# Kernel tuning notes

Hardware: AMD Instinct MI355X
Metric: run time of the kernel (lower is better)

The kernel has to match this reference:

```python
import math
import jax, jax.numpy as jnp
import numpy as np

N, L, C_IMG, D, FF, H, NL, V = 2, 1024, 512, 512, 2048, 8, 4, 8000
EPS_ATTN = 1e-6
EPS_LN = 1e-5


def pos_enc(position, channels):
    # position: (N, L, 1) float. channels assumed even here (256 / 512).
    num = channels // 2
    log_inc = math.log(10000.0) / (num - 1)
    inv = jnp.exp(jnp.arange(num, dtype=position.dtype) * -log_inc)
    st = position * inv.reshape(1, 1, -1)  # (N, L, num)
    return jnp.concatenate([jnp.sin(st), jnp.cos(st)], -1)


def layer_norm(x, s, b):
    m = jnp.mean(x, -1, keepdims=True)
    v = jnp.mean((x - m) ** 2, -1, keepdims=True)
    return (x - m) / jnp.sqrt(v + EPS_LN) * s + b


def causal_linear_attention(x, mask, Wq, bq, Wk, bk, Wv, bv, Wo, bo):
    # x: (N, L, D), mask: (N, L, 1)
    n, l, d = x.shape
    q = (x @ Wq + bq).reshape(n, l, H, -1)
    k = (x @ Wk + bk).reshape(n, l, H, -1)
    v = (x @ Wv + bv).reshape(n, l, H, -1)
    Q = jax.nn.elu(q) + 1.0                       # elu feature map
    K = (jax.nn.elu(k) + 1.0) * mask[:, :, :, None]
    K_cum = jnp.cumsum(K, axis=1)                 # (N, L, H, dk)
    Z = 1.0 / (jnp.einsum('nlhd,nlhd->nlh', Q, K_cum) + EPS_ATTN)
    KV = jnp.cumsum(K[..., :, None] * v[..., None, :], axis=1)  # (N, L, H, dk, dv)
    out = jnp.einsum('nlhd,nlhde->nlhe', Q, KV) * Z[..., None]
    return out.reshape(n, l, d) @ Wo + bo


def encoder_layer(x, mask, p):
    (Wq, bq, Wk, bk, Wv, bv, Wo, bo, W1, b1, W2, b2, s1, be1, s2, be2) = p
    x = x + causal_linear_attention(x, mask, Wq, bq, Wk, bk, Wv, bv, Wo, bo)
    x = layer_norm(x, s1, be1)
    y = jax.nn.gelu(x @ W1 + b1, approximate=False) @ W2 + b2
    return layer_norm(x + y, s2, be2)


def setup_inputs() -> dict:
    key = jax.random.key(0)
    ks = iter(jax.random.split(key, 64))

    def p(shape):
        return jax.random.normal(next(ks), shape, dtype=jnp.float32) * 0.02

    x_img = jax.random.normal(next(ks), (N, L, C_IMG), dtype=jnp.float32)
    x_txt = jax.random.randint(next(ks), (N, L), 0, V)
    pos = jnp.broadcast_to(jnp.arange(L, dtype=jnp.float32)[None, :, None], (N, L, 1))
    pos_r = jnp.floor(pos / 32.0)
    pos_c = jnp.mod(pos, 32.0)
    pos_t = pos
    first_half = (jnp.arange(L) < L // 2).astype(jnp.float32)[None, :, None]
    mask_img = jnp.broadcast_to(first_half, (N, L, 1))
    mask_txt = 1.0 - mask_img

    inp = dict(x_img=x_img, x_txt=x_txt, mask_img=mask_img, mask_txt=mask_txt,
               pos_r=pos_r, pos_c=pos_c, pos_t=pos_t,
               W_ei=p((C_IMG, D)), b_ei=jnp.zeros((D,)),
               emb_txt=p((V, D)),
               Wq=p((NL, D, D)), bq=jnp.zeros((NL, D)),
               Wk=p((NL, D, D)), bk=jnp.zeros((NL, D)),
               Wv=p((NL, D, D)), bv=jnp.zeros((NL, D)),
               Wo=p((NL, D, D)), bo=jnp.zeros((NL, D)),
               W1=p((NL, D, FF)), b1=jnp.zeros((NL, FF)),
               W2=p((NL, FF, D)), b2=jnp.zeros((NL, D)),
               ln1_s=jnp.ones((NL, D)), ln1_b=jnp.zeros((NL, D)),
               ln2_s=jnp.ones((NL, D)), ln2_b=jnp.zeros((NL, D)),
               W_pi=p((D, C_IMG)), b_pi=jnp.zeros((C_IMG,)),
               W_pt=p((D, V)), b_pt=jnp.zeros((V,)))
    return inp


def reference(x_img, x_txt, mask_img, mask_txt, pos_r, pos_c, pos_t,
              W_ei, b_ei, emb_txt,
              Wq, bq, Wk, bk, Wv, bv, Wo, bo, W1, b1, W2, b2,
              ln1_s, ln1_b, ln2_s, ln2_b, W_pi, b_pi, W_pt, b_pt):
    x_mask = mask_img + mask_txt  # (N, L, 1)
    # image embedding
    half = D // 2
    x_pos = jnp.concatenate([pos_enc(pos_r, half), pos_enc(pos_c, D - half)], -1)
    x_emb_img = ((x_img @ W_ei + b_ei) + x_pos) * mask_img
    # text embedding
    x_emb_txt = (emb_txt[x_txt] + pos_enc(pos_t, D)) * mask_txt
    x = x_emb_img + x_emb_txt
    for i in range(NL):
        p = (Wq[i], bq[i], Wk[i], bk[i], Wv[i], bv[i], Wo[i], bo[i],
             W1[i], b1[i], W2[i], b2[i], ln1_s[i], ln1_b[i], ln2_s[i], ln2_b[i])
        x = encoder_layer(x, x_mask, p)
    logit_img = x @ W_pi + b_pi
    logit_txt = x @ W_pt + b_pt
    return (logit_img, logit_txt)
```

## Files before the change

### kernel.cpp

```cpp
#include <hip/hip_runtime.h>
#include <hip/hip_bf16.h>
#include <math.h>

#define NB 2
#define LSEQ 1024
#define DM 512
#define FFD 2048
#define NHEAD 8
#define DKH 64
#define NLAYER 4
#define VOCAB 8000
#define NCHUNK 16
#define NROWS (NB * LSEQ)
#define QS 1536
#define NHEADCAT 8512
#define NHEADPAD 8576

#define OP_NONE 0
#define OP_GELU 2
#define OP_QKV  3
#define OP_PART 4
#define OP_HEAD 5

typedef __attribute__((ext_vector_type(8))) short short8;
typedef __attribute__((ext_vector_type(4))) float f32x4;
typedef __hip_bfloat16 bf16;

__device__ __forceinline__ void cast_tile(
    const float* __restrict__ s, bf16* __restrict__ d, int K, int N,
    int n0, int k0, int tid)
{
    __shared__ float tile[32][33];
    const int r  = tid >> 3;
    const int c4 = (tid & 7) * 4;
    const int n  = n0 + c4;
    float4 v = make_float4(0.f, 0.f, 0.f, 0.f);
    if (n < N)
        v = *(const float4*)(s + (size_t)(k0 + r) * N + n);
    tile[r][c4 + 0] = v.x; tile[r][c4 + 1] = v.y;
    tile[r][c4 + 2] = v.z; tile[r][c4 + 3] = v.w;
    __syncthreads();
    const int nr = tid >> 3;
    const int kc = (tid & 7) * 4;
    bf16 o[4];
    o[0] = __float2bfloat16(tile[kc + 0][nr]);
    o[1] = __float2bfloat16(tile[kc + 1][nr]);
    o[2] = __float2bfloat16(tile[kc + 2][nr]);
    o[3] = __float2bfloat16(tile[kc + 3][nr]);
    *(unsigned long long*)(d + (size_t)(n0 + nr) * K + k0 + kc) =
        *(const unsigned long long*)o;
    __syncthreads();
}

#define CO_QKVO 0
#define CO_W1   4096
#define CO_W2   8192
#define CO_WEI  12288
#define CO_WPI  12544
#define CO_WPT  12800
#define CO_XIMG 16832
#define CO_QKVB 17856
#define CO_HB   17860
#define CO_END  17894

__global__ __launch_bounds__(256) void setup_all(
    const float* __restrict__ Wq, const float* __restrict__ Wk,
    const float* __restrict__ Wv, const float* __restrict__ Wo,
    const float* __restrict__ W1, const float* __restrict__ W2,
    const float* __restrict__ Wei, const float* __restrict__ Wpi,
    const float* __restrict__ Wpt,
    bf16* __restrict__ QKVt, bf16* __restrict__ Wot,
    bf16* __restrict__ W1t, bf16* __restrict__ W2t,
    bf16* __restrict__ Weit, bf16* __restrict__ Whead,
    const float* __restrict__ x_img, bf16* __restrict__ ximgh,
    const float* __restrict__ bq, const float* __restrict__ bk,
    const float* __restrict__ bv, float* __restrict__ qkvB,
    const float* __restrict__ bpi, const float* __restrict__ bpt,
    float* __restrict__ hb)
{
    const int id = blockIdx.x;
    const int tid = threadIdx.x;

    if (id < CO_W1) {
        const int rel = id;
        const int z = rel >> 8, t = rel & 255;
        const int layer = z >> 2, which = z & 3;
        const float* src = (which == 0 ? Wq : which == 1 ? Wk : which == 2 ? Wv : Wo)
                           + (size_t)layer * 262144;
        bf16* dst = (which < 3)
            ? (QKVt + (size_t)layer * 786432 + (size_t)which * 262144)
            : (Wot + (size_t)layer * 262144);
        cast_tile(src, dst, 512, 512, (t & 15) * 32, (t >> 4) * 32, tid);
    } else if (id < CO_W2) {
        const int rel = id - CO_W1;
        const int z = rel >> 10, t = rel & 1023;
        cast_tile(W1 + (size_t)z * 1048576, W1t + (size_t)z * 1048576,
                  512, 2048, (t & 63) * 32, (t >> 6) * 32, tid);
    } else if (id < CO_WEI) {
        const int rel = id - CO_W2;
        const int z = rel >> 10, t = rel & 1023;
        cast_tile(W2 + (size_t)z * 1048576, W2t + (size_t)z * 1048576,
                  2048, 512, (t & 15) * 32, (t >> 4) * 32, tid);
    } else if (id < CO_WPI) {
        const int t = id - CO_WEI;
        cast_tile(Wei, Weit, 512, 512, (t & 15) * 32, (t >> 4) * 32, tid);
    } else if (id < CO_WPT) {
        const int t = id - CO_WPI;
        cast_tile(Wpi, Whead, 512, 512, (t & 15) * 32, (t >> 4) * 32, tid);
    } else if (id < CO_XIMG) {
        const int t = id - CO_WPT;
        cast_tile(Wpt, Whead + 262144, 512, VOCAB,
                  (t % 252) * 32, (t / 252) * 32, tid);
    } else if (id < CO_QKVB) {
        const int i = (id - CO_XIMG) * 256 + tid;
        const float4 v = *(const float4*)(x_img + (size_t)i * 4);
        ximgh[(size_t)i * 4 + 0] = __float2bfloat16(v.x);
        ximgh[(size_t)i * 4 + 1] = __float2bfloat16(v.y);
        ximgh[(size_t)i * 4 + 2] = __float2bfloat16(v.z);
        ximgh[(size_t)i * 4 + 3] = __float2bfloat16(v.w);
    } else if (id < CO_HB) {
        const int z = id - CO_QKVB;
        for (int j = tid; j < QS; j += 256) {
            float v;
            if (j < 512)       v = bq[z * DM + j];
            else if (j < 1024) v = bk[z * DM + j - 512];
            else               v = bv[z * DM + j - 1024];
            qkvB[z * QS + j] = v;
        }
    } else {
        const int j = (id - CO_HB) * 256 + tid;
        if (j < NHEADPAD)
            hb[j] = (j < 512) ? bpi[j] : (j < NHEADCAT ? bpt[j - 512] : 0.f);
    }
}

template<int BM, int BN>
__global__ __launch_bounds__(256) void gemm16(
    const bf16* __restrict__ A, const bf16* __restrict__ Bt,
    const float* __restrict__ bias, const float* __restrict__ res,
    float* __restrict__ outF, float* __restrict__ outF2,
    bf16* __restrict__ outH,
    int M, int K, int Nout, int op, int kslab)
{
    constexpr int WM = BM / 2, WN = BN / 2, MI = WM / 16, NI = WN / 16;
    constexpr int LA = BM / 64, LB = BN / 64;
    constexpr int NL = LA + LB;
    __shared__ bf16 As[3][BM * 32];
    __shared__ bf16 Bs[3][BN * 32];
    const int tid = threadIdx.x;
    const int lane = tid & 63;
    const int wave = tid >> 6;
    const int wm = (wave >> 1) * WM, wn = (wave & 1) * WN;

    int bxi = blockIdx.x, byi = blockIdx.y;
    if (op == OP_HEAD) {
        const int gx = gridDim.x;
        const int nwg = gx * gridDim.y;
        int flat = byi * gx + bxi;
        const int q = nwg >> 3, r = nwg & 7;
        const int xcd = flat & 7, lid = flat >> 3;
        flat = (xcd < r ? xcd * (q + 1) : r * (q + 1) + (xcd - r) * q) + lid;
        bxi = flat % gx;
        byi = flat / gx;
    }
    const int bm = (op == OP_HEAD ? bxi : blockIdx.y) * BM;
    const int bn = (op == OP_HEAD ? byi : blockIdx.x) * BN;
    const int l16 = lane & 15, quad = lane >> 4;

    const int rA = tid >> 2;
    const int c8 = (tid & 3) << 3;

    f32x4 acc[MI][NI];
    #pragma unroll
    for (int i = 0; i < MI; ++i)
        #pragma unroll
        for (int j = 0; j < NI; ++j) acc[i][j] = (f32x4){0.f, 0.f, 0.f, 0.f};

    const bf16* gA = A  + (size_t)(bm + rA) * K + c8;
    const bf16* gB = Bt + (size_t)(bn + rA) * K + c8;
    const int ldsWaveOff = wave * 1024;

    const int kStart = blockIdx.z * kslab;
    const int kEnd = kStart + kslab;

    auto stage = [&](int buf, int k0) {
        #pragma unroll
        for (int i = 0; i < LA; ++i)
            __builtin_amdgcn_global_load_lds(
                (const __attribute__((address_space(1))) void*)(gA + (size_t)i * 64 * K + k0),
                (__attribute__((address_space(3))) void*)((char*)As[buf] + i * 4096 + ldsWaveOff),
                16, 0, 0);
        #pragma unroll
        for (int i = 0; i < LB; ++i)
            __builtin_amdgcn_global_load_lds(
                (const __attribute__((address_space(1))) void*)(gB + (size_t)i * 64 * K + k0),
                (__attribute__((address_space(3))) void*)((char*)Bs[buf] + i * 4096 + ldsWaveOff),
                16, 0, 0);
    };

    stage(0, kStart);
    if (kStart + 32 < kEnd) stage(1, kStart + 32);
    int cur = 0;
    for (int k0 = kStart; k0 < kEnd; k0 += 32) {
        const int k2 = k0 + 64;
        if (k2 < kEnd) {
            int nb = cur + 2; if (nb >= 3) nb -= 3;
            stage(nb, k2);
            asm volatile("s_waitcnt vmcnt(%0)" :: "n"(2 * NL) : "memory");
        } else if (k0 + 32 < kEnd) {
            asm volatile("s_waitcnt vmcnt(%0)" :: "n"(NL) : "memory");
        } else {
            asm volatile("s_waitcnt vmcnt(0)" ::: "memory");
        }
        __builtin_amdgcn_s_barrier();
        short8 a[MI], b[NI];
        #pragma unroll
        for (int i = 0; i < MI; ++i)
            a[i] = *(const short8*)(As[cur] + (size_t)(wm + i * 16 + l16) * 32 + quad * 8);
        #pragma unroll
        for (int j = 0; j < NI; ++j)
            b[j] = *(const short8*)(Bs[cur] + (size_t)(wn + j * 16 + l16) * 32 + quad * 8);
        #pragma unroll
        for (int i = 0; i < MI; ++i)
            #pragma unroll
            for (int j = 0; j < NI; ++j)
                acc[i][j] = __builtin_amdgcn_mfma_f32_16x16x32_bf16(
                    a[i], b[j], acc[i][j], 0, 0, 0);
        __builtin_amdgcn_s_barrier();
        ++cur; if (cur >= 3) cur -= 3;
    }

    if (op == OP_PART) {
        float* dst = outF + (size_t)blockIdx.z * (size_t)M * Nout;
        #pragma unroll
        for (int j = 0; j < NI; ++j) {
            const int col = bn + wn + j * 16 + l16;
            #pragma unroll
            for (int i = 0; i < MI; ++i)
                #pragma unroll
                for (int r = 0; r < 4; ++r) {
                    const int row = bm + wm + i * 16 + quad * 4 + r;
                    dst[(size_t)row * Nout + col] = acc[i][j][r];
                }
        }
        return;
    }
    if (op == OP_HEAD) {
        #pragma unroll
        for (int j = 0; j < NI; ++j) {
            const int col = bn + wn + j * 16 + l16;
            const bool cok = (col < NHEADCAT);
            const float bz = cok ? bias[col] : 0.f;
            #pragma unroll
            for (int i = 0; i < MI; ++i)
                #pragma unroll
                for (int r = 0; r < 4; ++r) {
                    const int row = bm + wm + i * 16 + quad * 4 + r;
                    const float v = acc[i][j][r] + bz;
                    if (cok) {
                        if (col < 512) outF[(size_t)row * 512 + col] = v;
                        else           outF2[(size_t)row * VOCAB + (col - 512)] = v;
                    }
                }
        }
        return;
    }

    #pragma unroll
    for (int j = 0; j < NI; ++j) {
        const int col = bn + wn + j * 16 + l16;
        const bool cok = (col < Nout);
        const float bz = cok ? bias[col] : 0.f;
        #pragma unroll
        for (int i = 0; i < MI; ++i) {
            #pragma unroll
            for (int r = 0; r < 4; ++r) {
                const int row = bm + wm + i * 16 + quad * 4 + r;
                float v = acc[i][j][r] + bz;
                if (op == OP_GELU)      v = 0.5f * v * (1.f + erff(v * 0.70710678118654752f));
                else if (op == OP_QKV && col < 1024) v = (v > 0.f) ? v + 1.f : expf(v);
                if (cok) {
                    if (res)  v += res[(size_t)row * Nout + col];
                    if (outF) outF[(size_t)row * Nout + col] = v;
                    if (outH) outH[(size_t)row * Nout + col] = __float2bfloat16(v);
                }
            }
        }
    }
}

__global__ __launch_bounds__(256) void embed_k(
    const float* __restrict__ gI, const int* __restrict__ xt,
    const float* __restrict__ emb,
    const float* __restrict__ mi, const float* __restrict__ mt,
    const float* __restrict__ pr, const float* __restrict__ pc,
    const float* __restrict__ pt, float* __restrict__ X, bf16* __restrict__ Xh)
{
    const int row = blockIdx.x;
    const float prv = pr[row], pcv = pc[row], ptv = pt[row];
    const float miv = mi[row], mtv = mt[row];
    const int tok = xt[row];
    const float LOG1E4 = 9.2103403719761836f;
    const float LI127 = LOG1E4 / 127.f;
    const float LI255 = LOG1E4 / 255.f;

    for (int d = threadIdx.x; d < DM; d += 256) {
        float ip;
        if (d < 128)       ip = sinf(prv * expf(-(float)d * LI127));
        else if (d < 256)  ip = cosf(prv * expf(-(float)(d - 128) * LI127));
        else if (d < 384)  ip = sinf(pcv * expf(-(float)(d - 256) * LI127));
        else               ip = cosf(pcv * expf(-(float)(d - 384) * LI127));
        float tp;
        if (d < 256) tp = sinf(ptv * expf(-(float)d * LI255));
        else         tp = cosf(ptv * expf(-(float)(d - 256) * LI255));
        const float v = miv * (gI[(size_t)row * DM + d] + ip)
                      + mtv * (emb[(size_t)tok * DM + d] + tp);
        X[(size_t)row * DM + d] = v;
        Xh[(size_t)row * DM + d] = __float2bfloat16(v);
    }
}

__global__ __launch_bounds__(256) void ln_red(
    const float* __restrict__ P, int nP,
    const float* __restrict__ bias, const float* __restrict__ res,
    const float* __restrict__ g, const float* __restrict__ b,
    float* __restrict__ out, bf16* __restrict__ outh)
{
    const int row = blockIdx.x;
    const int tid = threadIdx.x;
    const int lane = tid & 63, wv = tid >> 6;
    const size_t base = (size_t)row * DM;
    float x0 = res[base + tid] + bias[tid];
    float x1 = res[base + tid + 256] + bias[tid + 256];
    for (int p = 0; p < nP; ++p) {
        x0 += P[(size_t)p * 1048576 + base + tid];
        x1 += P[(size_t)p * 1048576 + base + tid + 256];
    }
    __shared__ float redA[4];
    __shared__ float redB[4];
    float s = x0 + x1;
    #pragma unroll
    for (int off = 32; off > 0; off >>= 1) s += __shfl_down(s, off);
    if (lane == 0) redA[wv] = s;
    __syncthreads();
    const float mean = (redA[0] + redA[1] + redA[2] + redA[3]) * (1.f / (float)DM);
    const float d0 = x0 - mean, d1 = x1 - mean;
    float v = d0 * d0 + d1 * d1;
    #pragma unroll
    for (int off = 32; off > 0; off >>= 1) v += __shfl_down(v, off);
    if (lane == 0) redB[wv] = v;
    __syncthreads();
    const float var = (redB[0] + redB[1] + redB[2] + redB[3]) * (1.f / (float)DM);
    const float rstd = rsqrtf(var + 1e-5f);
    const float y0 = d0 * rstd * g[tid] + b[tid];
    const float y1 = d1 * rstd * g[tid + 256] + b[tid + 256];
    out[base + tid]        = y0;
    out[base + tid + 256]  = y1;
    outh[base + tid]       = __float2bfloat16(y0);
    outh[base + tid + 256] = __float2bfloat16(y1);
}

__global__ __launch_bounds__(256) void attn_kv(
    const float* __restrict__ Kp, const float* __restrict__ Vp,
    float* __restrict__ S, float* __restrict__ ks)
{
    const int c = blockIdx.x, h = blockIdx.y, n = blockIdx.z;
    const int tid = threadIdx.x;
    __shared__ float sK[64][64], sV[64][64], part[4][64];

    const int lr = tid >> 4;
    const int c4 = (tid & 15) * 4;
    #pragma unroll
    for (int it = 0; it < 4; ++it) {
        const int row = it * 16 + lr;
        const size_t gb = ((size_t)(n * LSEQ + c * 64 + row)) * QS + h * DKH + c4;
        *(float4*)&sK[row][c4] = *(const float4*)(Kp + gb);
        *(float4*)&sV[row][c4] = *(const float4*)(Vp + gb);
    }
    __syncthreads();

    const int e = tid & 63, dq = tid >> 6;
    float s[16] = {};
    for (int l = 0; l < 64; ++l) {
        const float vv = sV[l][e];
        const float4 k0 = *(const float4*)&sK[l][dq * 16 + 0];
        const float4 k1 = *(const float4*)&sK[l][dq * 16 + 4];
        const float4 k2 = *(const float4*)&sK[l][dq * 16 + 8];
        const float4 k3 = *(const float4*)&sK[l][dq * 16 + 12];
        s[0]  = fmaf(k0.x, vv, s[0]);  s[1]  = fmaf(k0.y, vv, s[1]);
        s[2]  = fmaf(k0.z, vv, s[2]);  s[3]  = fmaf(k0.w, vv, s[3]);
        s[4]  = fmaf(k1.x, vv, s[4]);  s[5]  = fmaf(k1.y, vv, s[5]);
        s[6]  = fmaf(k1.z, vv, s[6]);  s[7]  = fmaf(k1.w, vv, s[7]);
        s[8]  = fmaf(k2.x, vv, s[8]);  s[9]  = fmaf(k2.y, vv, s[9]);
        s[10] = fmaf(k2.z, vv, s[10]); s[11] = fmaf(k2.w, vv, s[11]);
        s[12] = fmaf(k3.x, vv, s[12]); s[13] = fmaf(k3.y, vv, s[13]);
        s[14] = fmaf(k3.z, vv, s[14]); s[15] = fmaf(k3.w, vv, s[15]);
    }
    const size_t sb = (((size_t)(n * NHEAD + h)) * NCHUNK + c) * 4096;
    #pragma unroll
    for (int i = 0; i < 16; ++i) S[sb + (size_t)(dq * 16 + i) * 64 + e] = s[i];

    float kp = 0.f;
    #pragma unroll
    for (int i = 0; i < 16; ++i) kp += sK[dq * 16 + i][e];
    part[dq][e] = kp;
    __syncthreads();
    if (tid < 64)
        ks[(((size_t)(n * NHEAD + h)) * NCHUNK + c) * 64 + tid] =
            part[0][tid] + part[1][tid] + part[2][tid] + part[3][tid];
}

__global__ __launch_bounds__(256) void attn_out(
    const float* __restrict__ QKV, const float* __restrict__ S,
    const float* __restrict__ ks, bf16* __restrict__ O)
{
    const int c = blockIdx.x, h = blockIdx.y, n = blockIdx.z;
    const int tid = threadIdx.x;
    __shared__ float sQt[64][64];
    __shared__ float sKt[64][64];
    __shared__ float sV [64][64];
    __shared__ float sS [64][64];
    __shared__ float sPt[64][65];
    __shared__ float skp[64];

    const size_t nhS = ((size_t)(n * NHEAD + h)) * NCHUNK * 4096;
    const size_t nhK = ((size_t)(n * NHEAD + h)) * NCHUNK * 64;

    {
        float4 aS[4] = {};
        for (int cc = 0; cc < c; ++cc) {
            const float* Sc = S + nhS + (size_t)cc * 4096;
            #pragma unroll
            for (int i = 0; i < 4; ++i) {
                const float4 t = *(const float4*)(Sc + i * 1024 + tid * 4);
                aS[i].x += t.x; aS[i].y += t.y; aS[i].z += t.z; aS[i].w += t.w;
            }
        }
        float* sSf = &sS[0][0];
        #pragma unroll
        for (int i = 0; i < 4; ++i)
            *(float4*)(sSf + i * 1024 + tid * 4) = aS[i];
        if (tid < 64) {
            float kp = 0.f;
            for (int cc = 0; cc < c; ++cc) kp += ks[nhK + cc * 64 + tid];
            skp[tid] = kp;
        }
    }

    const int lr = tid >> 4;
    const int c4 = (tid & 15) * 4;
    #pragma unroll
    for (int it = 0; it < 4; ++it) {
        const int row = it * 16 + lr;
        const size_t gb = ((size_t)(n * LSEQ + c * 64 + row)) * QS + h * DKH + c4;
        const float4 q4 = *(const float4*)(QKV + gb);
        const float4 k4 = *(const float4*)(QKV + gb + 512);
        const float4 v4 = *(const float4*)(QKV + gb + 1024);
        sQt[c4 + 0][row] = q4.x; sQt[c4 + 1][row] = q4.y;
        sQt[c4 + 2][row] = q4.z; sQt[c4 + 3][row] = q4.w;
        sKt[c4 + 0][row] = k4.x; sKt[c4 + 1][row] = k4.y;
        sKt[c4 + 2][row] = k4.z; sKt[c4 + 3][row] = k4.w;
        *(float4*)&sV[row][c4] = v4;
    }
    __syncthreads();

    const int m4 = (tid & 15) * 4;
    const int lg = tid >> 4;
    {
        float p[4][4] = {};
        for (int d = 0; d < 64; ++d) {
            const float4 k4 = *(const float4*)&sKt[d][m4];
            const float4 q4 = *(const float4*)&sQt[d][lg * 4];
            p[0][0] = fmaf(q4.x, k4.x, p[0][0]); p[0][1] = fmaf(q4.x, k4.y, p[0][1]);
            p[0][2] = fmaf(q4.x, k4.z, p[0][2]); p[0][3] = fmaf(q4.x, k4.w, p[0][3]);
            p[1][0] = fmaf(q4.y, k4.x, p[1][0]); p[1][1] = fmaf(q4.y, k4.y, p[1][1]);
            p[1][2] = fmaf(q4.y, k4.z, p[1][2]); p[1][3] = fmaf(q4.y, k4.w, p[1][3]);
            p[2][0] = fmaf(q4.z, k4.x, p[2][0]); p[2][1] = fmaf(q4.z, k4.y, p[2][1]);
            p[2][2] = fmaf(q4.z, k4.z, p[2][2]); p[2][3] = fmaf(q4.z, k4.w, p[2][3]);
            p[3][0] = fmaf(q4.w, k4.x, p[3][0]); p[3][1] = fmaf(q4.w, k4.y, p[3][1]);
            p[3][2] = fmaf(q4.w, k4.z, p[3][2]); p[3][3] = fmaf(q4.w, k4.w, p[3][3]);
        }
        #pragma unroll
        for (int jj = 0; jj < 4; ++jj)
            #pragma unroll
            for (int j = 0; j < 4; ++j)
                sPt[m4 + jj][lg * 4 + j] = p[j][jj];
    }
    __syncthreads();

    float acc[4][4] = {};
    float z[4] = {};
    const int lmax = lg * 4 + 3;
    for (int m = 0; m <= lmax; ++m) {
        const float4 v4 = *(const float4*)&sV[m][m4];
        #pragma unroll
        for (int j = 0; j < 4; ++j) {
            const int l = lg * 4 + j;
            float p = sPt[m][l];
            p = (m <= l) ? p : 0.f;
            z[j] += p;
            acc[j][0] = fmaf(p, v4.x, acc[j][0]);
            acc[j][1] = fmaf(p, v4.y, acc[j][1]);
            acc[j][2] = fmaf(p, v4.z, acc[j][2]);
            acc[j][3] = fmaf(p, v4.w, acc[j][3]);
        }
    }
    for (int d = 0; d < 64; ++d) {
        const float4 s4 = *(const float4*)&sS[d][m4];
        const float4 q4 = *(const float4*)&sQt[d][lg * 4];
        const float kp = skp[d];
        z[0] = fmaf(q4.x, kp, z[0]); z[1] = fmaf(q4.y, kp, z[1]);
        z[2] = fmaf(q4.z, kp, z[2]); z[3] = fmaf(q4.w, kp, z[3]);
        acc[0][0] = fmaf(q4.x, s4.x, acc[0][0]); acc[0][1] = fmaf(q4.x, s4.y, acc[0][1]);
        acc[0][2] = fmaf(q4.x, s4.z, acc[0][2]); acc[0][3] = fmaf(q4.x, s4.w, acc[0][3]);
        acc[1][0] = fmaf(q4.y, s4.x, acc[1][0]); acc[1][1] = fmaf(q4.y, s4.y, acc[1][1]);
        acc[1][2] = fmaf(q4.y, s4.z, acc[1][2]); acc[1][3] = fmaf(q4.y, s4.w, acc[1][3]);
        acc[2][0] = fmaf(q4.z, s4.x, acc[2][0]); acc[2][1] = fmaf(q4.z, s4.y, acc[2][1]);
        acc[2][2] = fmaf(q4.z, s4.z, acc[2][2]); acc[2][3] = fmaf(q4.z, s4.w, acc[2][3]);
        acc[3][0] = fmaf(q4.w, s4.x, acc[3][0]); acc[3][1] = fmaf(q4.w, s4.y, acc[3][1]);
        acc[3][2] = fmaf(q4.w, s4.z, acc[3][2]); acc[3][3] = fmaf(q4.w, s4.w, acc[3][3]);
    }
    #pragma unroll
    for (int j = 0; j < 4; ++j) {
        const int l = lg * 4 + j;
        const float rz = 1.f / (z[j] + 1e-6f);
        const size_t ob = ((size_t)(n * LSEQ + c * 64 + l)) * DM + h * DKH + m4;
        O[ob + 0] = __float2bfloat16(acc[j][0] * rz);
        O[ob + 1] = __float2bfloat16(acc[j][1] * rz);
        O[ob + 2] = __float2bfloat16(acc[j][2] * rz);
        O[ob + 3] = __float2bfloat16(acc[j][3] * rz);
    }
}

extern "C" void kernel_launch(void* const* d_in, const int* in_sizes, int n_in,
                              void* d_out, int out_size, void* d_ws, size_t ws_size,
                              hipStream_t stream)
{
    const float* x_img   = (const float*)d_in[0];
    const int*   x_txt   = (const int*)  d_in[1];
    const float* mask_i  = (const float*)d_in[2];
    const float* mask_t  = (const float*)d_in[3];
    const float* pos_r   = (const float*)d_in[4];
    const float* pos_c   = (const float*)d_in[5];
    const float* pos_t   = (const float*)d_in[6];
    const float* W_ei    = (const float*)d_in[7];
    const float* b_ei    = (const float*)d_in[8];
    const float* emb_txt = (const float*)d_in[9];
    const float* Wq      = (const float*)d_in[10];
    const float* bq      = (const float*)d_in[11];
    const float* Wk      = (const float*)d_in[12];
    const float* bk      = (const float*)d_in[13];
    const float* Wv      = (const float*)d_in[14];
    const float* bv      = (const float*)d_in[15];
    const float* Wo      = (const float*)d_in[16];
    const float* bo      = (const float*)d_in[17];
    const float* W1      = (const float*)d_in[18];
    const float* b1      = (const float*)d_in[19];
    const float* W2      = (const float*)d_in[20];
    const float* b2      = (const float*)d_in[21];
    const float* ln1_s   = (const float*)d_in[22];
    const float* ln1_b   = (const float*)d_in[23];
    const float* ln2_s   = (const float*)d_in[24];
    const float* ln2_b   = (const float*)d_in[25];
    const float* W_pi    = (const float*)d_in[26];
    const float* b_pi    = (const float*)d_in[27];
    const float* W_pt    = (const float*)d_in[28];
    const float* b_pt    = (const float*)d_in[29];

    float* ws = (float*)d_ws;
    size_t off = 0;
    auto alloc = [&](size_t nfloats) { float* p = ws + off; off += nfloats; return p; };

    float* Xb   = alloc(1048576);
    float* Pb   = alloc(4194304);
    float* QKVb = alloc(3145728);
    float* Sb   = alloc(1048576);
    float* ksb  = alloc(16384);
    float* qkvB = alloc(4 * QS);
    float* hb   = alloc(8704);
    bf16* Xh    = (bf16*)alloc(524288);
    bf16* Ob    = (bf16*)alloc(524288);
    bf16* Tb    = (bf16*)alloc(2097152);
    bf16* ximgh = (bf16*)alloc(524288);
    bf16* QKVt  = (bf16*)alloc(1572864);
    bf16* Wot   = (bf16*)alloc(524288);
    bf16* W1t   = (bf16*)alloc(2097152);
    bf16* W2t   = (bf16*)alloc(2097152);
    bf16* Weit  = (bf16*)alloc(131072);
    bf16* Whead = (bf16*)alloc(2195456);

    const dim3 blk(256);
    const dim3 gAttn(NCHUNK, NHEAD, NB);

    setup_all<<<dim3(CO_END), blk, 0, stream>>>(
        Wq, Wk, Wv, Wo, W1, W2, W_ei, W_pi, W_pt,
        QKVt, Wot, W1t, W2t, Weit, Whead,
        x_img, ximgh, bq, bk, bv, qkvB, b_pi, b_pt, hb);

    gemm16<64, 64><<<dim3(8, 32), blk, 0, stream>>>(
        ximgh, Weit, b_ei, nullptr, Pb, nullptr, nullptr, NROWS, 512, 512, OP_NONE, 512);
    embed_k<<<NROWS, blk, 0, stream>>>(Pb, x_txt, emb_txt, mask_i, mask_t,
                                       pos_r, pos_c, pos_t, Xb, Xh);

    for (int i = 0; i < NLAYER; ++i) {
        gemm16<64, 128><<<dim3(12, 32), blk, 0, stream>>>(
            Xh, QKVt + (size_t)i * 786432, qkvB + i * QS, nullptr,
            QKVb, nullptr, nullptr, NROWS, 512, QS, OP_QKV, 512);

        attn_kv<<<gAttn, blk, 0, stream>>>(QKVb + 512, QKVb + 1024, Sb, ksb);
        attn_out<<<gAttn, blk, 0, stream>>>(QKVb, Sb, ksb, Ob);

        gemm16<64, 64><<<dim3(8, 32, 2), blk, 0, stream>>>(
            Ob, Wot + (size_t)i * 262144, nullptr, nullptr,
            Pb, nullptr, nullptr, NROWS, 512, 512, OP_PART, 256);
        ln_red<<<NROWS, blk, 0, stream>>>(Pb, 2, bo + (size_t)i * DM, Xb,
                                          ln1_s + (size_t)i * DM,
                                          ln1_b + (size_t)i * DM, Xb, Xh);

        gemm16<64, 128><<<dim3(16, 32), blk, 0, stream>>>(
            Xh, W1t + (size_t)i * 1048576, b1 + (size_t)i * FFD, nullptr,
            nullptr, nullptr, Tb, NROWS, 512, FFD, OP_GELU, 512);
        gemm16<64, 64><<<dim3(8, 32, 4), blk, 0, stream>>>(
            Tb, W2t + (size_t)i * 1048576, nullptr, nullptr,
            Pb, nullptr, nullptr, NROWS, 2048, 512, OP_PART, 512);
        ln_red<<<NROWS, blk, 0, stream>>>(Pb, 4, b2 + (size_t)i * DM, Xb,
                                          ln2_s + (size_t)i * DM,
                                          ln2_b + (size_t)i * DM, Xb, Xh);
    }

    float* out = (float*)d_out;
    gemm16<128, 128><<<dim3(16, 67), blk, 0, stream>>>(
        Xh, Whead, hb, nullptr, out, out + 1048576, nullptr,
        NROWS, 512, NHEADCAT, OP_HEAD, 512);
}
```

Measured before the change: 631.1 us.

## Fuse QKV projection with per-chunk KV state computation; use double-buffered GEMM

Adds a qkv_attn kernel in which each block computes the Q/K/V projection for one head and one 64-row chunk. It keeps K and V in shared memory and directly produces the chunk KV outer-product sums and K sums, so the separate attn_kv launch and its reload of K/V from global memory go away. To support this, the QKV weights and biases are re-laid out per head. The generic GEMM also moves from a triple-buffered to a double-buffered LDS pipeline, and the unused residual argument is removed. The fused kernel launches only 256 blocks, with a narrow per-block N tile, which may underuse the GPU compared with the old 384-block GEMM.

```diff
diff --git a/kernel.cpp b/kernel.cpp
--- a/kernel.cpp
+++ b/kernel.cpp
@@ -18,7 +18,6 @@
 
 #define OP_NONE 0
 #define OP_GELU 2
-#define OP_QKV  3
 #define OP_PART 4
 #define OP_HEAD 5
 
@@ -87,10 +86,15 @@
         const int layer = z >> 2, which = z & 3;
         const float* src = (which == 0 ? Wq : which == 1 ? Wk : which == 2 ? Wv : Wo)
                            + (size_t)layer * 262144;
-        bf16* dst = (which < 3)
-            ? (QKVt + (size_t)layer * 786432 + (size_t)which * 262144)
-            : (Wot + (size_t)layer * 262144);
-        cast_tile(src, dst, 512, 512, (t & 15) * 32, (t >> 4) * 32, tid);
+        const int n0 = (t & 15) * 32, k0 = (t >> 4) * 32;
+        if (which < 3) {
+            const int h = n0 >> 6;
+            bf16* dst = QKVt + (size_t)layer * 786432
+                      + (size_t)(h * 128 + which * 64) * 512;
+            cast_tile(src, dst, 512, 512, n0, k0, tid);
+        } else {
+            cast_tile(src, Wot + (size_t)layer * 262144, 512, 512, n0, k0, tid);
+        }
     } else if (id < CO_W2) {
         const int rel = id - CO_W1;
         const int z = rel >> 10, t = rel & 1023;
@@ -121,11 +125,10 @@
     } else if (id < CO_HB) {
         const int z = id - CO_QKVB;
         for (int j = tid; j < QS; j += 256) {
-            float v;
-            if (j < 512)       v = bq[z * DM + j];
-            else if (j < 1024) v = bk[z * DM + j - 512];
-            else               v = bv[z * DM + j - 1024];
-            qkvB[z * QS + j] = v;
+            const int h = j / 192, rem = j - h * 192;
+            const int which = rem >> 6, idx = rem & 63;
+            const float* bsrc = (which == 0 ? bq : which == 1 ? bk : bv);
+            qkvB[z * QS + j] = bsrc[z * DM + h * 64 + idx];
         }
     } else {
         const int j = (id - CO_HB) * 256 + tid;
@@ -137,7 +140,7 @@
 template<int BM, int BN>
 __global__ __launch_bounds__(256) void gemm16(
     const bf16* __restrict__ A, const bf16* __restrict__ Bt,
-    const float* __restrict__ bias, const float* __restrict__ res,
+    const float* __restrict__ bias,
     float* __restrict__ outF, float* __restrict__ outF2,
     bf16* __restrict__ outH,
     int M, int K, int Nout, int op, int kslab)
@@ -145,8 +148,8 @@
     constexpr int WM = BM / 2, WN = BN / 2, MI = WM / 16, NI = WN / 16;
     constexpr int LA = BM / 64, LB = BN / 64;
     constexpr int NL = LA + LB;
-    __shared__ bf16 As[3][BM * 32];
-    __shared__ bf16 Bs[3][BN * 32];
+    __shared__ bf16 As[2][BM * 32];
+    __shared__ bf16 Bs[2][BN * 32];
     const int tid = threadIdx.x;
     const int lane = tid & 63;
     const int wave = tid >> 6;
@@ -199,15 +202,11 @@
     };
 
     stage(0, kStart);
-    if (kStart + 32 < kEnd) stage(1, kStart + 32);
     int cur = 0;
     for (int k0 = kStart; k0 < kEnd; k0 += 32) {
-        const int k2 = k0 + 64;
-        if (k2 < kEnd) {
-            int nb = cur + 2; if (nb >= 3) nb -= 3;
-            stage(nb, k2);
-            asm volatile("s_waitcnt vmcnt(%0)" :: "n"(2 * NL) : "memory");
-        } else if (k0 + 32 < kEnd) {
+        const bool hasNext = (k0 + 32 < kEnd);
+        if (hasNext) {
+            stage(cur ^ 1, k0 + 32);
             asm volatile("s_waitcnt vmcnt(%0)" :: "n"(NL) : "memory");
         } else {
             asm volatile("s_waitcnt vmcnt(0)" ::: "memory");
@@ -227,7 +226,7 @@
                 acc[i][j] = __builtin_amdgcn_mfma_f32_16x16x32_bf16(
                     a[i], b[j], acc[i][j], 0, 0, 0);
         __builtin_amdgcn_s_barrier();
-        ++cur; if (cur >= 3) cur -= 3;
+        cur ^= 1;
     }
 
     if (op == OP_PART) {
@@ -277,16 +276,142 @@
             for (int r = 0; r < 4; ++r) {
                 const int row = bm + wm + i * 16 + quad * 4 + r;
                 float v = acc[i][j][r] + bz;
-                if (op == OP_GELU)      v = 0.5f * v * (1.f + erff(v * 0.70710678118654752f));
-                else if (op == OP_QKV && col < 1024) v = (v > 0.f) ? v + 1.f : expf(v);
+                if (op == OP_GELU) v = 0.5f * v * (1.f + erff(v * 0.70710678118654752f));
                 if (cok) {
-                    if (res)  v += res[(size_t)row * Nout + col];
                     if (outF) outF[(size_t)row * Nout + col] = v;
                     if (outH) outH[(size_t)row * Nout + col] = __float2bfloat16(v);
                 }
             }
         }
     }
+}
+
+__global__ __launch_bounds__(256) void qkv_attn(
+    const bf16* __restrict__ A, const bf16* __restrict__ Bt,
+    const float* __restrict__ bias,
+    float* __restrict__ QKVb, float* __restrict__ S, float* __restrict__ ks)
+{
+    __shared__ char smem[33792];
+    const int c = blockIdx.x, h = blockIdx.y, n = blockIdx.z;
+    const int tid = threadIdx.x;
+    const int lane = tid & 63;
+    const int wave = tid >> 6;
+    const int l16 = lane & 15, quad = lane >> 4;
+    const int r0 = n * LSEQ + c * 64;
+    const int wn = wave * 48;
+
+    const bf16* Bh = Bt + (size_t)(h * 192) * 512;
+    const float* bh = bias + h * 192;
+
+    f32x4 acc[4][3];
+    #pragma unroll
+    for (int i = 0; i < 4; ++i)
+        #pragma unroll
+        for (int j = 0; j < 3; ++j) acc[i][j] = (f32x4){0.f, 0.f, 0.f, 0.f};
+
+    const bf16* gA = A + (size_t)(r0 + (tid >> 2)) * 512 + ((tid & 3) << 3);
+    const int ldsWaveOff = wave * 1024;
+
+    auto stage = [&](int buf, int k0) {
+        __builtin_amdgcn_global_load_lds(
+            (const __attribute__((address_space(1))) void*)(gA + k0),
+            (__attribute__((address_space(3))) void*)(smem + buf * 4096 + ldsWaveOff),
+            16, 0, 0);
+        #pragma unroll
+        for (int p = 0; p < 3; ++p)
+            __builtin_amdgcn_global_load_lds(
+                (const __attribute__((address_space(1))) void*)(
+                    Bh + (size_t)(p * 64 + (tid >> 2)) * 512 + ((tid & 3) << 3) + k0),
+                (__attribute__((address_space(3))) void*)(
+                    smem + 8192 + buf * 12288 + p * 4096 + ldsWaveOff),
+                16, 0, 0);
+    };
+
+    stage(0, 0);
+    int cur = 0;
+    for (int k0 = 0; k0 < 512; k0 += 32) {
+        if (k0 + 32 < 512) {
+            stage(cur ^ 1, k0 + 32);
+            asm volatile("s_waitcnt vmcnt(4)" ::: "memory");
+        } else {
+            asm volatile("s_waitcnt vmcnt(0)" ::: "memory");
+        }
+        __builtin_amdgcn_s_barrier();
+        const bf16* Asb = (const bf16*)(smem + cur * 4096);
+        const bf16* Bsb = (const bf16*)(smem + 8192 + cur * 12288);
+        short8 a[4], b[3];
+        #pragma unroll
+        for (int i = 0; i < 4; ++i)
+            a[i] = *(const short8*)(Asb + (i * 16 + l16) * 32 + quad * 8);
+        #pragma unroll
+        for (int j = 0; j < 3; ++j)
+            b[j] = *(const short8*)(Bsb + (wn + j * 16 + l16) * 32 + quad * 8);
+        #pragma unroll
+        for (int i = 0; i < 4; ++i)
+            #pragma unroll
+            for (int j = 0; j < 3; ++j)
+                acc[i][j] = __builtin_amdgcn_mfma_f32_16x16x32_bf16(
+                    a[i], b[j], acc[i][j], 0, 0, 0);
+        __builtin_amdgcn_s_barrier();
+        cur ^= 1;
+    }
+    __syncthreads();
+
+    float* sK   = (float*)smem;
+    float* sV   = (float*)(smem + 16384);
+    float* part = (float*)(smem + 32768);
+
+    #pragma unroll
+    for (int j = 0; j < 3; ++j) {
+        const int col = wn + j * 16 + l16;
+        const float bz = bh[col];
+        int gcol;
+        if (col < 64)        gcol = h * 64 + col;
+        else if (col < 128)  gcol = 512 + h * 64 + (col - 64);
+        else                 gcol = 1024 + h * 64 + (col - 128);
+        #pragma unroll
+        for (int i = 0; i < 4; ++i)
+            #pragma unroll
+            for (int r = 0; r < 4; ++r) {
+                const int row = i * 16 + quad * 4 + r;
+                float v = acc[i][j][r] + bz;
+                if (col < 128) v = (v > 0.f) ? v + 1.f : expf(v);
+                QKVb[(size_t)(r0 + row) * QS + gcol] = v;
+                if (col >= 128)     sV[row * 64 + (col - 128)] = v;
+                else if (col >= 64) sK[row * 64 + (col - 64)]  = v;
+            }
+    }
+    __syncthreads();
+
+    const int e = tid & 63, dq = tid >> 6;
+    float s[16] = {};
+    for (int l = 0; l < 64; ++l) {
+        const float vv = sV[l * 64 + e];
+        const float4 k0v = *(const float4*)(sK + l * 64 + dq * 16 + 0);
+        const float4 k1v = *(const float4*)(sK + l * 64 + dq * 16 + 4);
+        const float4 k2v = *(const float4*)(sK + l * 64 + dq * 16 + 8);
+        const float4 k3v = *(const float4*)(sK + l * 64 + dq * 16 + 12);
+        s[0]  = fmaf(k0v.x, vv, s[0]);  s[1]  = fmaf(k0v.y, vv, s[1]);
+        s[2]  = fmaf(k0v.z, vv, s[2]);  s[3]  = fmaf(k0v.w, vv, s[3]);
+        s[4]  = fmaf(k1v.x, vv, s[4]);  s[5]  = fmaf(k1v.y, vv, s[5]);
+        s[6]  = fmaf(k1v.z, vv, s[6]);  s[7]  = fmaf(k1v.w, vv, s[7]);
+        s[8]  = fmaf(k2v.x, vv, s[8]);  s[9]  = fmaf(k2v.y, vv, s[9]);
+        s[10] = fmaf(k2v.z, vv, s[10]); s[11] = fmaf(k2v.w, vv, s[11]);
+        s[12] = fmaf(k3v.x, vv, s[12]); s[13] = fmaf(k3v.y, vv, s[13]);
+        s[14] = fmaf(k3v.z, vv, s[14]); s[15] = fmaf(k3v.w, vv, s[15]);
+    }
+    const size_t sb = (((size_t)(n * NHEAD + h)) * NCHUNK + c) * 4096;
+    #pragma unroll
+    for (int i = 0; i < 16; ++i) S[sb + (size_t)(dq * 16 + i) * 64 + e] = s[i];
+
+    float kp = 0.f;
+    #pragma unroll
+    for (int i = 0; i < 16; ++i) kp += sK[(dq * 16 + i) * 64 + e];
+    part[dq * 64 + e] = kp;
+    __syncthreads();
+    if (tid < 64)
+        ks[(((size_t)(n * NHEAD + h)) * NCHUNK + c) * 64 + tid] =
+            part[tid] + part[64 + tid] + part[128 + tid] + part[192 + tid];
 }
 
 __global__ __launch_bounds__(256) void embed_k(
@@ -358,56 +483,6 @@
     out[base + tid + 256]  = y1;
     outh[base + tid]       = __float2bfloat16(y0);
     outh[base + tid + 256] = __float2bfloat16(y1);
-}
-
-__global__ __launch_bounds__(256) void attn_kv(
-    const float* __restrict__ Kp, const float* __restrict__ Vp,
-    float* __restrict__ S, float* __restrict__ ks)
-{
-    const int c = blockIdx.x, h = blockIdx.y, n = blockIdx.z;
-    const int tid = threadIdx.x;
-    __shared__ float sK[64][64], sV[64][64], part[4][64];
-
-    const int lr = tid >> 4;
-    const int c4 = (tid & 15) * 4;
-    #pragma unroll
-    for (int it = 0; it < 4; ++it) {
-        const int row = it * 16 + lr;
-        const size_t gb = ((size_t)(n * LSEQ + c * 64 + row)) * QS + h * DKH + c4;
-        *(float4*)&sK[row][c4] = *(const float4*)(Kp + gb);
-        *(float4*)&sV[row][c4] = *(const float4*)(Vp + gb);
-    }
-    __syncthreads();
-
-    const int e = tid & 63, dq = tid >> 6;
-    float s[16] = {};
-    for (int l = 0; l < 64; ++l) {
-        const float vv = sV[l][e];
-        const float4 k0 = *(const float4*)&sK[l][dq * 16 + 0];
-        const float4 k1 = *(const float4*)&sK[l][dq * 16 + 4];
-        const float4 k2 = *(const float4*)&sK[l][dq * 16 + 8];
-        const float4 k3 = *(const float4*)&sK[l][dq * 16 + 12];
-        s[0]  = fmaf(k0.x, vv, s[0]);  s[1]  = fmaf(k0.y, vv, s[1]);
-        s[2]  = fmaf(k0.z, vv, s[2]);  s[3]  = fmaf(k0.w, vv, s[3]);
-        s[4]  = fmaf(k1.x, vv, s[4]);  s[5]  = fmaf(k1.y, vv, s[5]);
-        s[6]  = fmaf(k1.z, vv, s[6]);  s[7]  = fmaf(k1.w, vv, s[7]);
-        s[8]  = fmaf(k2.x, vv, s[8]);  s[9]  = fmaf(k2.y, vv, s[9]);
-        s[10] = fmaf(k2.z, vv, s[10]); s[11] = fmaf(k2.w, vv, s[11]);
-        s[12] = fmaf(k3.x, vv, s[12]); s[13] = fmaf(k3.y, vv, s[13]);
-        s[14] = fmaf(k3.z, vv, s[14]); s[15] = fmaf(k3.w, vv, s[15]);
-    }
-    const size_t sb = (((size_t)(n * NHEAD + h)) * NCHUNK + c) * 4096;
-    #pragma unroll
-    for (int i = 0; i < 16; ++i) S[sb + (size_t)(dq * 16 + i) * 64 + e] = s[i];
-
-    float kp = 0.f;
-    #pragma unroll
-    for (int i = 0; i < 16; ++i) kp += sK[dq * 16 + i][e];
-    part[dq][e] = kp;
-    __syncthreads();
-    if (tid < 64)
-        ks[(((size_t)(n * NHEAD + h)) * NCHUNK + c) * 64 + tid] =
-            part[0][tid] + part[1][tid] + part[2][tid] + part[3][tid];
 }
 
 __global__ __launch_bounds__(256) void attn_out(
@@ -598,30 +673,28 @@
         x_img, ximgh, bq, bk, bv, qkvB, b_pi, b_pt, hb);
 
     gemm16<64, 64><<<dim3(8, 32), blk, 0, stream>>>(
-        ximgh, Weit, b_ei, nullptr, Pb, nullptr, nullptr, NROWS, 512, 512, OP_NONE, 512);
+        ximgh, Weit, b_ei, Pb, nullptr, nullptr, NROWS, 512, 512, OP_NONE, 512);
     embed_k<<<NROWS, blk, 0, stream>>>(Pb, x_txt, emb_txt, mask_i, mask_t,
                                        pos_r, pos_c, pos_t, Xb, Xh);
 
     for (int i = 0; i < NLAYER; ++i) {
-        gemm16<64, 128><<<dim3(12, 32), blk, 0, stream>>>(
-            Xh, QKVt + (size_t)i * 786432, qkvB + i * QS, nullptr,
-            QKVb, nullptr, nullptr, NROWS, 512, QS, OP_QKV, 512);
-
-        attn_kv<<<gAttn, blk, 0, stream>>>(QKVb + 512, QKVb + 1024, Sb, ksb);
+        qkv_attn<<<gAttn, blk, 0, stream>>>(
+            Xh, QKVt + (size_t)i * 786432, qkvB + i * QS, QKVb, Sb, ksb);
+
         attn_out<<<gAttn, blk, 0, stream>>>(QKVb, Sb, ksb, Ob);
 
         gemm16<64, 64><<<dim3(8, 32, 2), blk, 0, stream>>>(
-            Ob, Wot + (size_t)i * 262144, nullptr, nullptr,
+            Ob, Wot + (size_t)i * 262144, nullptr,
             Pb, nullptr, nullptr, NROWS, 512, 512, OP_PART, 256);
         ln_red<<<NROWS, blk, 0, stream>>>(Pb, 2, bo + (size_t)i * DM, Xb,
                                           ln1_s + (size_t)i * DM,
                                           ln1_b + (size_t)i * DM, Xb, Xh);
 
         gemm16<64, 128><<<dim3(16, 32), blk, 0, stream>>>(
-            Xh, W1t + (size_t)i * 1048576, b1 + (size_t)i * FFD, nullptr,
+            Xh, W1t + (size_t)i * 1048576, b1 + (size_t)i * FFD,
             nullptr, nullptr, Tb, NROWS, 512, FFD, OP_GELU, 512);
         gemm16<64, 64><<<dim3(8, 32, 4), blk, 0, stream>>>(
-            Tb, W2t + (size_t)i * 1048576, nullptr, nullptr,
+            Tb, W2t + (size_t)i * 1048576, nullptr,
             Pb, nullptr, nullptr, NROWS, 2048, 512, OP_PART, 512);
         ln_red<<<NROWS, blk, 0, stream>>>(Pb, 4, b2 + (size_t)i * DM, Xb,
                                           ln2_s + (size_t)i * DM,
@@ -630,6 +703,6 @@
 
     float* out = (float*)d_out;
     gemm16<128, 128><<<dim3(16, 67), blk, 0, stream>>>(
-        Xh, Whead, hb, nullptr, out, out + 1048576, nullptr,
+        Xh, Whead, hb, out, out + 1048576, nullptr,
         NROWS, 512, NHEADCAT, OP_HEAD, 512);
 }
```

Measured after the change: 609.2 us. 3.5% less time.
